# Kernel tuning notes

Hardware: AMD Instinct MI355X
Metric: run time of the kernel (lower is better)

## Reference

```python
import jax, jax.numpy as jnp
import numpy as np

N, E, IN_DIM, HID, OUT = 50000, 600000, 128, 256, 128

def setup_inputs() -> dict:
    key = jax.random.key(0)
    k1, k2, k3, k4, k5, k6, k7 = jax.random.split(key, 7)
    h = jax.random.normal(k1, (N, IN_DIM), dtype=jnp.float32)
    src = jax.random.randint(k2, (E,), 0, N)
    dst = jax.random.randint(k3, (E,), 0, N)
    s1 = 1.0 / np.sqrt(2 * IN_DIM)
    s2 = 1.0 / np.sqrt(HID)
    W1 = jax.random.uniform(k4, (2 * IN_DIM, HID), minval=-s1, maxval=s1, dtype=jnp.float32)
    b1 = jax.random.uniform(k5, (HID,), minval=-s1, maxval=s1, dtype=jnp.float32)
    W2 = jax.random.uniform(k6, (HID, OUT), minval=-s2, maxval=s2, dtype=jnp.float32)
    b2 = jax.random.uniform(k7, (OUT,), minval=-s2, maxval=s2, dtype=jnp.float32)
    return {"h": h, "src": src, "dst": dst, "W1": W1, "b1": b1, "W2": W2, "b2": b2}

def reference(h, src, dst, W1, b1, W2, b2):
    n = h.shape[0]
    # copy_u + mean: gather src features, segment-sum at dst, divide by in-degree
    msg_sum = jax.ops.segment_sum(h[src], dst, num_segments=n)          # [N, D]
    deg = jax.ops.segment_sum(jnp.ones((src.shape[0],), h.dtype), dst, num_segments=n)
    h_neigh = msg_sum / jnp.maximum(deg, 1.0)[:, None]                  # zero-deg nodes -> 0
    h_total = jnp.concatenate([h, h_neigh], axis=1)                     # [N, 2D]
    out = (h_total @ W1 + b1) @ W2 + b2                                 # 2-layer MLP (no inner activation)
    return jax.nn.relu(out)
```

## Files before the change

### kernel.cpp

```cpp
#include <hip/hip_runtime.h>

#define N_NODES 50000
#define E_EDGES 600000
#define IN_DIM  128
#define HID     256
#define OUT_DIM 128
#define CAP     64

#define RANGE_N 6250
#define CHUNK_E 2048
#define NB_FILL 2344
#define NB_HCVT 3125
#define NB_WCVT 384
#define NB_CVT  (NB_HCVT + NB_WCVT)
#define NB_MLP  782

typedef __bf16 bf16x8 __attribute__((ext_vector_type(8)));
typedef float  f32x16 __attribute__((ext_vector_type(16)));
typedef unsigned short ushort8 __attribute__((ext_vector_type(8)));

__device__ __forceinline__ unsigned short f2bf(float f) {
    union { float f; unsigned int i; } v; v.f = f;
    unsigned int b = v.i;
    b += 0x7fffu + ((b >> 16) & 1u);
    return (unsigned short)(b >> 16);
}
__device__ __forceinline__ void acc2(unsigned u, float& a0, float& a1) {
    union { unsigned i; float f; } lo, hi;
    lo.i = u << 16; hi.i = u & 0xffff0000u;
    a0 += lo.f; a1 += hi.f;
}

__global__ void __launch_bounds__(256)
sage_fill(const int* __restrict__ src, const int* __restrict__ dst,
          int* __restrict__ counts, char* __restrict__ outb) {
    int b = blockIdx.x;
    int r = b & 7;
    int chunk = b >> 3;
    int e0 = chunk * CHUNK_E + threadIdx.x * 8;
    if (e0 < E_EDGES) {
        int lo = r * RANGE_N, hi = lo + RANGE_N;
        const int4 d0 = *(const int4*)(dst + e0);
        const int4 d1 = *(const int4*)(dst + e0 + 4);
        int dd[8] = {d0.x, d0.y, d0.z, d0.w, d1.x, d1.y, d1.z, d1.w};
        #pragma unroll
        for (int k = 0; k < 8; ++k) {
            int d = dd[k];
            if (d >= lo && d < hi) {
                int s = src[e0 + k];
                int sl = atomicAdd(counts + d, 1);
                if (sl < CAP) *((int*)(outb + (size_t)d * 512 + 256) + sl) = s;
            }
        }
    }
}

__global__ void __launch_bounds__(256)
sage_cvt(const float* __restrict__ h, unsigned short* __restrict__ ht,
         const float* __restrict__ W1, const float* __restrict__ W2,
         unsigned short* __restrict__ w1sw, unsigned short* __restrict__ w2sw) {
    int b = blockIdx.x;
    if (b < NB_HCVT) {
        int idx = b * 256 + threadIdx.x;
        int n = idx >> 4, g = idx & 15;
        const float4 v0 = *(const float4*)(h + (size_t)n * IN_DIM + g * 8);
        const float4 v1 = *(const float4*)(h + (size_t)n * IN_DIM + g * 8 + 4);
        ushort8 o;
        o[0] = f2bf(v0.x); o[1] = f2bf(v0.y); o[2] = f2bf(v0.z); o[3] = f2bf(v0.w);
        o[4] = f2bf(v1.x); o[5] = f2bf(v1.y); o[6] = f2bf(v1.z); o[7] = f2bf(v1.w);
        *(ushort8*)(ht + (size_t)n * 128 + g * 8) = o;
    } else {
        int i1 = (b - NB_HCVT) * 256 + threadIdx.x;
        if (i1 < 65536) {
            int j = i1 & 7, n = (i1 >> 3) & 255, g = (i1 >> 11) & 1, ks = (i1 >> 12) & 3, c = i1 >> 14;
            int k = c * 64 + ks * 16 + g * 8 + j;
            w1sw[i1] = f2bf(W1[(size_t)k * HID + n]);
        } else {
            int i2 = i1 - 65536;
            int j = i2 & 7, n = (i2 >> 3) & 127, g = (i2 >> 10) & 1, ks = (i2 >> 11) & 7, c = (i2 >> 14) & 1;
            int k = c * 128 + ks * 16 + g * 8 + j;
            w2sw[i2] = f2bf(W2[(size_t)k * OUT_DIM + n]);
        }
    }
}

__global__ void __launch_bounds__(256, 4)
sage_fused(const int* __restrict__ counts,
           const unsigned short* __restrict__ ht,
           const unsigned short* __restrict__ w1sw,
           const unsigned short* __restrict__ w2sw,
           const float* __restrict__ b1,
           const float* __restrict__ b2,
           float* out) {
    __shared__ unsigned short hid_s[64][264];

    const int t = threadIdx.x;
    const int nw = t >> 6;
    const int lane = t & 63;
    const int lr = lane & 31;
    const int lg = lane >> 5;
    const int base = blockIdx.x * 64;
    const int row0 = min(base + lr,      N_NODES - 1);
    const int row1 = min(base + 32 + lr, N_NODES - 1);

    {
        #pragma unroll 1
        for (int g = 0; g < 4; ++g) {
            const int m0 = nw * 16 + g * 4;
            float a0[4], a1[4];
            int deg[4], ent[4];
            const int* bk[4];
            int4 q[4];
            int em = 0;
            #pragma unroll
            for (int j = 0; j < 4; ++j) {
                a0[j] = 0.f; a1[j] = 0.f;
                int node = min(base + m0 + j, N_NODES - 1);
                deg[j] = __builtin_amdgcn_readfirstlane(counts[node]);
                ent[j] = min(deg[j], CAP);
                em = max(em, ent[j]);
                bk[j] = (const int*)((const char*)out + (size_t)node * 512 + 256);
                q[j] = *(const int4*)(bk[j]);
            }
            #pragma unroll 1
            for (int p = 0; p < em; p += 4) {
                int4 nx[4];
                #pragma unroll
                for (int j = 0; j < 4; ++j)
                    nx[j] = *(const int4*)(bk[j] + min(p + 4, CAP - 4));
                unsigned uu[16];
                #pragma unroll
                for (int k = 0; k < 4; ++k) {
                    #pragma unroll
                    for (int j = 0; j < 4; ++j) {
                        if (p + k < ent[j]) {
                            int idx = (k == 0) ? q[j].x : (k == 1) ? q[j].y
                                    : (k == 2) ? q[j].z : q[j].w;
                            idx = __builtin_amdgcn_readfirstlane(idx);
                            uu[k * 4 + j] = *(const unsigned*)(ht + (size_t)idx * 128 + lane * 2);
                        }
                    }
                }
                #pragma unroll
                for (int k = 0; k < 4; ++k) {
                    #pragma unroll
                    for (int j = 0; j < 4; ++j) {
                        if (p + k < ent[j])
                            acc2(uu[k * 4 + j], a0[j], a1[j]);
                    }
                }
                #pragma unroll
                for (int j = 0; j < 4; ++j) q[j] = nx[j];
            }
            #pragma unroll
            for (int j = 0; j < 4; ++j) {
                float inv = 1.0f / (float)max(deg[j], 1);
                unsigned o = (unsigned)f2bf(a0[j] * inv) | ((unsigned)f2bf(a1[j] * inv) << 16);
                *(unsigned*)(&hid_s[m0 + j][lane * 2]) = o;
            }
        }
    }

    f32x16 c1[2][2];
    #pragma unroll
    for (int e2 = 0; e2 < 16; ++e2) {
        c1[0][0][e2] = 0.f; c1[0][1][e2] = 0.f; c1[1][0][e2] = 0.f; c1[1][1][e2] = 0.f;
    }

    #pragma unroll
    for (int c = 0; c < 2; ++c) {
        bf16x8 a0[4], a1[4];
        #pragma unroll
        for (int ks = 0; ks < 4; ++ks) {
            int koff = (c * 4 + ks) * 16 + lg * 8;
            a0[ks] = *(const bf16x8*)(ht + (size_t)row0 * 128 + koff);
            a1[ks] = *(const bf16x8*)(ht + (size_t)row1 * 128 + koff);
        }
        #pragma unroll
        for (int ks = 0; ks < 4; ++ks) {
            #pragma unroll
            for (int nt = 0; nt < 2; ++nt) {
                int n = nw * 64 + nt * 32 + lr;
                bf16x8 b = *(const bf16x8*)(w1sw + c * 16384 + (((ks * 2 + lg) * 256) + n) * 8);
                c1[0][nt] = __builtin_amdgcn_mfma_f32_32x32x16_bf16(a0[ks], b, c1[0][nt], 0, 0, 0);
                c1[1][nt] = __builtin_amdgcn_mfma_f32_32x32x16_bf16(a1[ks], b, c1[1][nt], 0, 0, 0);
            }
        }
    }

    __syncthreads();

    #pragma unroll
    for (int c = 2; c < 4; ++c) {
        bf16x8 a0[4], a1[4];
        #pragma unroll
        for (int ks = 0; ks < 4; ++ks) {
            int koff = (c - 2) * 64 + ks * 16 + lg * 8;
            a0[ks] = *(const bf16x8*)(&hid_s[lr][koff]);
            a1[ks] = *(const bf16x8*)(&hid_s[32 + lr][koff]);
        }
        #pragma unroll
        for (int ks = 0; ks < 4; ++ks) {
            #pragma unroll
            for (int nt = 0; nt < 2; ++nt) {
                int n = nw * 64 + nt * 32 + lr;
                bf16x8 b = *(const bf16x8*)(w1sw + c * 16384 + (((ks * 2 + lg) * 256) + n) * 8);
                c1[0][nt] = __builtin_amdgcn_mfma_f32_32x32x16_bf16(a0[ks], b, c1[0][nt], 0, 0, 0);
                c1[1][nt] = __builtin_amdgcn_mfma_f32_32x32x16_bf16(a1[ks], b, c1[1][nt], 0, 0, 0);
            }
        }
    }

    __syncthreads();

    #pragma unroll
    for (int nt = 0; nt < 2; ++nt) {
        int col = nw * 64 + nt * 32 + lr;
        float bias = b1[col];
        #pragma unroll
        for (int s = 0; s < 2; ++s) {
            #pragma unroll
            for (int reg = 0; reg < 16; ++reg) {
                int m = s * 32 + (reg & 3) + 8 * (reg >> 2) + 4 * lg;
                hid_s[m][col] = f2bf(c1[s][nt][reg] + bias);
            }
        }
    }
    __syncthreads();

    f32x16 c2[2];
    #pragma unroll
    for (int e2 = 0; e2 < 16; ++e2) { c2[0][e2] = 0.f; c2[1][e2] = 0.f; }

    #pragma unroll
    for (int c = 0; c < 2; ++c) {
        #pragma unroll
        for (int ks = 0; ks < 8; ++ks) {
            bf16x8 b = *(const bf16x8*)(w2sw + c * 16384 + ((ks * 2 + lg) * 128 + nw * 32 + lr) * 8);
            int koff = c * 128 + ks * 16 + lg * 8;
            bf16x8 ah0 = *(const bf16x8*)(&hid_s[lr][koff]);
            bf16x8 ah1 = *(const bf16x8*)(&hid_s[32 + lr][koff]);
            c2[0] = __builtin_amdgcn_mfma_f32_32x32x16_bf16(ah0, b, c2[0], 0, 0, 0);
            c2[1] = __builtin_amdgcn_mfma_f32_32x32x16_bf16(ah1, b, c2[1], 0, 0, 0);
        }
    }

    {
        int col = nw * 32 + lr;
        float bias = b2[col];
        #pragma unroll
        for (int s = 0; s < 2; ++s) {
            #pragma unroll
            for (int reg = 0; reg < 16; ++reg) {
                int m = s * 32 + (reg & 3) + 8 * (reg >> 2) + 4 * lg;
                int n = base + m;
                if (n < N_NODES)
                    out[(size_t)n * OUT_DIM + col] = fmaxf(c2[s][reg] + bias, 0.0f);
            }
        }
    }
}

extern "C" void kernel_launch(void* const* d_in, const int* in_sizes, int n_in,
                              void* d_out, int out_size, void* d_ws, size_t ws_size,
                              hipStream_t stream) {
    const float* h   = (const float*)d_in[0];
    const int*   src = (const int*)d_in[1];
    const int*   dst = (const int*)d_in[2];
    const float* W1  = (const float*)d_in[3];
    const float* b1  = (const float*)d_in[4];
    const float* W2  = (const float*)d_in[5];
    const float* b2  = (const float*)d_in[6];
    float* out = (float*)d_out;

    int* counts = (int*)d_ws;
    unsigned short* w1sw = (unsigned short*)(counts + N_NODES);
    unsigned short* w2sw = w1sw + 65536;
    unsigned short* ht   = w2sw + 32768;

    hipMemsetAsync(counts, 0, N_NODES * sizeof(int), stream);

    sage_fill<<<NB_FILL, 256, 0, stream>>>(src, dst, counts, (char*)d_out);

    sage_cvt<<<NB_CVT, 256, 0, stream>>>(h, ht, W1, W2, w1sw, w2sw);

    sage_fused<<<NB_MLP, 256, 0, stream>>>(counts, ht, w1sw, w2sw, b1, b2, out);
}
```

Measured before the change: 177.7 us.

## Merge fill and convert kernels; branchless gather via zero row; stage self features in LDS

Combines the edge-bucketing kernel and the bf16 conversion kernel into one launch so they run concurrently and one launch gap is removed. Adds a zero row to the bf16 feature table so masked neighbor loads become unconditional loads of zeros, which removes divergent branches in the gather loop. Self features are now copied into LDS during the aggregation phase and both halves of the first GEMM read A from LDS. The cost is extra loads of the zero row for padded slots, and the self-feature GEMM can no longer overlap the aggregation before the barrier. The zero row relies on the workspace having room past N_NODES.

```diff
diff --git a/kernel.cpp b/kernel.cpp
--- a/kernel.cpp
+++ b/kernel.cpp
@@ -6,13 +6,14 @@
 #define HID     256
 #define OUT_DIM 128
 #define CAP     64
+#define ZROW    N_NODES
 
 #define RANGE_N 6250
 #define CHUNK_E 2048
 #define NB_FILL 2344
 #define NB_HCVT 3125
 #define NB_WCVT 384
-#define NB_CVT  (NB_HCVT + NB_WCVT)
+#define NB_PREP (NB_FILL + NB_HCVT + NB_WCVT + 1)
 #define NB_MLP  782
 
 typedef __bf16 bf16x8 __attribute__((ext_vector_type(8)));
@@ -32,36 +33,33 @@
 }
 
 __global__ void __launch_bounds__(256)
-sage_fill(const int* __restrict__ src, const int* __restrict__ dst,
-          int* __restrict__ counts, char* __restrict__ outb) {
+sage_prep(const int* __restrict__ src, const int* __restrict__ dst,
+          int* __restrict__ counts, char* __restrict__ outb,
+          const float* __restrict__ h, unsigned short* __restrict__ ht,
+          const float* __restrict__ W1, const float* __restrict__ W2,
+          unsigned short* __restrict__ w1sw, unsigned short* __restrict__ w2sw) {
     int b = blockIdx.x;
-    int r = b & 7;
-    int chunk = b >> 3;
-    int e0 = chunk * CHUNK_E + threadIdx.x * 8;
-    if (e0 < E_EDGES) {
-        int lo = r * RANGE_N, hi = lo + RANGE_N;
-        const int4 d0 = *(const int4*)(dst + e0);
-        const int4 d1 = *(const int4*)(dst + e0 + 4);
-        int dd[8] = {d0.x, d0.y, d0.z, d0.w, d1.x, d1.y, d1.z, d1.w};
-        #pragma unroll
-        for (int k = 0; k < 8; ++k) {
-            int d = dd[k];
-            if (d >= lo && d < hi) {
-                int s = src[e0 + k];
-                int sl = atomicAdd(counts + d, 1);
-                if (sl < CAP) *((int*)(outb + (size_t)d * 512 + 256) + sl) = s;
-            }
-        }
-    }
-}
-
-__global__ void __launch_bounds__(256)
-sage_cvt(const float* __restrict__ h, unsigned short* __restrict__ ht,
-         const float* __restrict__ W1, const float* __restrict__ W2,
-         unsigned short* __restrict__ w1sw, unsigned short* __restrict__ w2sw) {
-    int b = blockIdx.x;
-    if (b < NB_HCVT) {
-        int idx = b * 256 + threadIdx.x;
+    if (b < NB_FILL) {
+        int r = b & 7;
+        int chunk = b >> 3;
+        int e0 = chunk * CHUNK_E + threadIdx.x * 8;
+        if (e0 < E_EDGES) {
+            int lo = r * RANGE_N, hi = lo + RANGE_N;
+            const int4 d0 = *(const int4*)(dst + e0);
+            const int4 d1 = *(const int4*)(dst + e0 + 4);
+            int dd[8] = {d0.x, d0.y, d0.z, d0.w, d1.x, d1.y, d1.z, d1.w};
+            #pragma unroll
+            for (int k = 0; k < 8; ++k) {
+                int d = dd[k];
+                if (d >= lo && d < hi) {
+                    int s = src[e0 + k];
+                    int sl = atomicAdd(counts + d, 1);
+                    if (sl < CAP) *((int*)(outb + (size_t)d * 512 + 256) + sl) = s;
+                }
+            }
+        }
+    } else if (b < NB_FILL + NB_HCVT) {
+        int idx = (b - NB_FILL) * 256 + threadIdx.x;
         int n = idx >> 4, g = idx & 15;
         const float4 v0 = *(const float4*)(h + (size_t)n * IN_DIM + g * 8);
         const float4 v1 = *(const float4*)(h + (size_t)n * IN_DIM + g * 8 + 4);
@@ -69,8 +67,8 @@
         o[0] = f2bf(v0.x); o[1] = f2bf(v0.y); o[2] = f2bf(v0.z); o[3] = f2bf(v0.w);
         o[4] = f2bf(v1.x); o[5] = f2bf(v1.y); o[6] = f2bf(v1.z); o[7] = f2bf(v1.w);
         *(ushort8*)(ht + (size_t)n * 128 + g * 8) = o;
-    } else {
-        int i1 = (b - NB_HCVT) * 256 + threadIdx.x;
+    } else if (b < NB_FILL + NB_HCVT + NB_WCVT) {
+        int i1 = (b - NB_FILL - NB_HCVT) * 256 + threadIdx.x;
         if (i1 < 65536) {
             int j = i1 & 7, n = (i1 >> 3) & 255, g = (i1 >> 11) & 1, ks = (i1 >> 12) & 3, c = i1 >> 14;
             int k = c * 64 + ks * 16 + g * 8 + j;
@@ -81,6 +79,9 @@
             int k = c * 128 + ks * 16 + g * 8 + j;
             w2sw[i2] = f2bf(W2[(size_t)k * OUT_DIM + n]);
         }
+    } else {
+        if (threadIdx.x < 64)
+            *(unsigned*)(ht + (size_t)ZROW * 128 + threadIdx.x * 2) = 0u;
     }
 }
 
@@ -100,8 +101,6 @@
     const int lr = lane & 31;
     const int lg = lane >> 5;
     const int base = blockIdx.x * 64;
-    const int row0 = min(base + lr,      N_NODES - 1);
-    const int row1 = min(base + 32 + lr, N_NODES - 1);
 
     {
         #pragma unroll 1
@@ -121,6 +120,8 @@
                 em = max(em, ent[j]);
                 bk[j] = (const int*)((const char*)out + (size_t)node * 512 + 256);
                 q[j] = *(const int4*)(bk[j]);
+                unsigned self = *(const unsigned*)(ht + (size_t)node * 128 + lane * 2);
+                *(unsigned*)(&hid_s[m0 + j][128 + lane * 2]) = self;
             }
             #pragma unroll 1
             for (int p = 0; p < em; p += 4) {
@@ -133,21 +134,18 @@
                 for (int k = 0; k < 4; ++k) {
                     #pragma unroll
                     for (int j = 0; j < 4; ++j) {
-                        if (p + k < ent[j]) {
-                            int idx = (k == 0) ? q[j].x : (k == 1) ? q[j].y
-                                    : (k == 2) ? q[j].z : q[j].w;
-                            idx = __builtin_amdgcn_readfirstlane(idx);
-                            uu[k * 4 + j] = *(const unsigned*)(ht + (size_t)idx * 128 + lane * 2);
-                        }
+                        int idx = (k == 0) ? q[j].x : (k == 1) ? q[j].y
+                                : (k == 2) ? q[j].z : q[j].w;
+                        idx = __builtin_amdgcn_readfirstlane(idx);
+                        idx = (p + k < ent[j]) ? idx : ZROW;
+                        uu[k * 4 + j] = *(const unsigned*)(ht + (size_t)idx * 128 + lane * 2);
                     }
                 }
                 #pragma unroll
                 for (int k = 0; k < 4; ++k) {
                     #pragma unroll
-                    for (int j = 0; j < 4; ++j) {
-                        if (p + k < ent[j])
-                            acc2(uu[k * 4 + j], a0[j], a1[j]);
-                    }
+                    for (int j = 0; j < 4; ++j)
+                        acc2(uu[k * 4 + j], a0[j], a1[j]);
                 }
                 #pragma unroll
                 for (int j = 0; j < 4; ++j) q[j] = nx[j];
@@ -161,6 +159,8 @@
         }
     }
 
+    __syncthreads();
+
     f32x16 c1[2][2];
     #pragma unroll
     for (int e2 = 0; e2 < 16; ++e2) {
@@ -168,34 +168,12 @@
     }
 
     #pragma unroll
-    for (int c = 0; c < 2; ++c) {
+    for (int c = 0; c < 4; ++c) {
         bf16x8 a0[4], a1[4];
         #pragma unroll
         for (int ks = 0; ks < 4; ++ks) {
-            int koff = (c * 4 + ks) * 16 + lg * 8;
-            a0[ks] = *(const bf16x8*)(ht + (size_t)row0 * 128 + koff);
-            a1[ks] = *(const bf16x8*)(ht + (size_t)row1 * 128 + koff);
-        }
-        #pragma unroll
-        for (int ks = 0; ks < 4; ++ks) {
-            #pragma unroll
-            for (int nt = 0; nt < 2; ++nt) {
-                int n = nw * 64 + nt * 32 + lr;
-                bf16x8 b = *(const bf16x8*)(w1sw + c * 16384 + (((ks * 2 + lg) * 256) + n) * 8);
-                c1[0][nt] = __builtin_amdgcn_mfma_f32_32x32x16_bf16(a0[ks], b, c1[0][nt], 0, 0, 0);
-                c1[1][nt] = __builtin_amdgcn_mfma_f32_32x32x16_bf16(a1[ks], b, c1[1][nt], 0, 0, 0);
-            }
-        }
-    }
-
-    __syncthreads();
-
-    #pragma unroll
-    for (int c = 2; c < 4; ++c) {
-        bf16x8 a0[4], a1[4];
-        #pragma unroll
-        for (int ks = 0; ks < 4; ++ks) {
-            int koff = (c - 2) * 64 + ks * 16 + lg * 8;
+            int koff = (c < 2) ? (128 + c * 64 + ks * 16 + lg * 8)
+                               : ((c - 2) * 64 + ks * 16 + lg * 8);
             a0[ks] = *(const bf16x8*)(&hid_s[lr][koff]);
             a1[ks] = *(const bf16x8*)(&hid_s[32 + lr][koff]);
         }
@@ -280,9 +258,8 @@
 
     hipMemsetAsync(counts, 0, N_NODES * sizeof(int), stream);
 
-    sage_fill<<<NB_FILL, 256, 0, stream>>>(src, dst, counts, (char*)d_out);
-
-    sage_cvt<<<NB_CVT, 256, 0, stream>>>(h, ht, W1, W2, w1sw, w2sw);
+    sage_prep<<<NB_PREP, 256, 0, stream>>>(
+        src, dst, counts, (char*)d_out, h, ht, W1, W2, w1sw, w2sw);
 
     sage_fused<<<NB_MLP, 256, 0, stream>>>(counts, ht, w1sw, w2sw, b1, b2, out);
 }
```

After: 169.6 us. 1.05x faster.
